# Performance work log

Hardware: AMD Instinct MI355X
Metric: run time of the kernel (lower is better)

Reference implementation:

```python
import jax, jax.numpy as jnp
import numpy as np

DIM = 256
N_EMBED = 8192
DECAY = 0.99
EPS = 1e-05


def setup_inputs() -> dict:
    key = jax.random.key(0)
    k1, k2, k3, k4 = jax.random.split(key, 4)
    z = jax.random.normal(k1, (16, 32, 32, DIM), dtype=jnp.float32)
    embedding = jax.random.normal(k2, (DIM, N_EMBED), dtype=jnp.float32)
    cluster_size = jax.random.uniform(k3, (N_EMBED,), dtype=jnp.float32)
    embedding_avg = jax.random.normal(k4, (DIM, N_EMBED), dtype=jnp.float32)
    return {"z": z, "embedding": embedding, "cluster_size": cluster_size,
            "embedding_avg": embedding_avg}


def reference(z, embedding, cluster_size, embedding_avg):
    flatten = z.reshape(-1, DIM)  # [N, dim]
    dist = ((flatten ** 2).sum(1, keepdims=True)
            - 2.0 * flatten @ embedding
            + (embedding ** 2).sum(0, keepdims=True))
    embed_ind_flat = jnp.argmin(dist, axis=1)  # [N] int
    embed_ind = embed_ind_flat.reshape(z.shape[:-1])
    # Gather codes: embedding is [dim, n_embed]; quantize [..., dim]
    quantize = jnp.take(embedding.T, embed_ind_flat, axis=0).reshape(z.shape)

    # EMA codebook update (training path), via segment sums (no dense one-hot)
    onehot_sum = jax.ops.segment_sum(
        jnp.ones_like(embed_ind_flat, dtype=flatten.dtype),
        embed_ind_flat, num_segments=N_EMBED)  # [n_embed]
    embed_sum = jax.ops.segment_sum(flatten, embed_ind_flat,
                                    num_segments=N_EMBED).T  # [dim, n_embed]
    new_cluster_size = cluster_size * DECAY + (1.0 - DECAY) * onehot_sum
    new_embedding_avg = embedding_avg * DECAY + (1.0 - DECAY) * embed_sum
    n = new_cluster_size.sum()
    smoothed = (new_cluster_size + EPS) / (n + N_EMBED * EPS) * n
    new_embedding = new_embedding_avg / smoothed[None, :]

    diff = jnp.mean((jax.lax.stop_gradient(quantize) - z) ** 2)
    quantize_st = z + jax.lax.stop_gradient(quantize - z)
    return (quantize_st, diff, embed_ind, new_embedding,
            new_cluster_size, new_embedding_avg)
```

## Files before the change

kernel.cpp:

```cpp
#include <hip/hip_runtime.h>


#define DIMC  256
#define NEMB  8192
#define NROWS 16384

#define OUT_Q      0u
#define OUT_DIFF   4194304u
#define OUT_IDX    4194305u
#define OUT_NEWEMB 4210689u
#define OUT_NEWCS  6307841u
#define OUT_NEWAVG 6316033u

#define WS_EHI    0u
#define WS_ELO    1048576u
#define WS_COUNT  2097152u
#define WS_DIFF   2105344u
#define WS_N      2105345u
#define WS_ENORM  2105346u
#define WS_PACK   2113540u

typedef __attribute__((ext_vector_type(8))) short short8;
typedef __attribute__((ext_vector_type(4))) float f32x4;

__device__ inline void split_bf16(float x, unsigned short& h, unsigned short& l) {
  unsigned u = __float_as_uint(x);
  unsigned r = u + 0x7FFFu + ((u >> 16) & 1u);
  h = (unsigned short)(r >> 16);
  float hf = __uint_as_float((unsigned)h << 16);
  float lo = x - hf;
  unsigned u2 = __float_as_uint(lo);
  unsigned r2 = u2 + 0x7FFFu + ((u2 >> 16) & 1u);
  l = (unsigned short)(r2 >> 16);
}

__device__ inline float bf16_f(unsigned short u) {
  return __uint_as_float((unsigned)u << 16);
}

__global__ __launch_bounds__(256) void prep_kernel(
    const float* __restrict__ z, const float* __restrict__ emb,
    const float* __restrict__ cs, unsigned short* __restrict__ z_hi,
    unsigned short* __restrict__ z_lo, unsigned short* __restrict__ e_hi,
    unsigned short* __restrict__ e_lo, float* __restrict__ enorm,
    float* __restrict__ embsum, unsigned long long* __restrict__ pack,
    float* __restrict__ count_diff, float* __restrict__ n_out) {
  const int b = blockIdx.x;
  const int t = threadIdx.x;
  __shared__ float tile[64][68];
  __shared__ float red[4][64];

  if (b < 1024) {
#pragma unroll
    for (int it = 0; it < 4; ++it) {
      const int idx = (b * 256 + t) + it * 262144;
      const float4 v = reinterpret_cast<const float4*>(z)[idx];
      ushort4 h, l;
      split_bf16(v.x, h.x, l.x);
      split_bf16(v.y, h.y, l.y);
      split_bf16(v.z, h.z, l.z);
      split_bf16(v.w, h.w, l.w);
      reinterpret_cast<ushort4*>(z_hi)[idx] = h;
      reinterpret_cast<ushort4*>(z_lo)[idx] = l;
    }
  } else if (b < 1536) {
    const int bb = b - 1024;
    const int n0 = (bb & 127) * 64;
    const int k0 = (bb >> 7) * 64;
    const int c4 = (t & 15) * 4;
    const int rr = t >> 4;
#pragma unroll
    for (int i = 0; i < 4; ++i) {
      const int kl = rr + i * 16;
      const float4 v = *reinterpret_cast<const float4*>(
          &emb[(size_t)(k0 + kl) * NEMB + n0 + c4]);
      *reinterpret_cast<float4*>(&tile[kl][c4]) = v;
    }
    __syncthreads();
#pragma unroll
    for (int i = 0; i < 4; ++i) {
      const int nr = rr + i * 16;
      float4 v;
      v.x = tile[c4 + 0][nr];
      v.y = tile[c4 + 1][nr];
      v.z = tile[c4 + 2][nr];
      v.w = tile[c4 + 3][nr];
      const size_t off = (size_t)(n0 + nr) * DIMC + k0 + c4;
      ushort4 h, l;
      split_bf16(v.x, h.x, l.x);
      split_bf16(v.y, h.y, l.y);
      split_bf16(v.z, h.z, l.z);
      split_bf16(v.w, h.w, l.w);
      *reinterpret_cast<ushort4*>(&e_hi[off]) = h;
      *reinterpret_cast<ushort4*>(&e_lo[off]) = l;
    }
  } else if (b < 2048) {
    const int bb = b - 1536;
    const float4 zero = {0.f, 0.f, 0.f, 0.f};
#pragma unroll
    for (int it = 0; it < 4; ++it)
      reinterpret_cast<float4*>(embsum)[bb * 1024 + t + it * 256] = zero;
  } else if (b < 2176) {
    const int l = t & 63;
    const int dg = t >> 6;
    const int e = (b - 2048) * 64 + l;
    float s = 0.f;
#pragma unroll 8
    for (int d = dg * 64; d < dg * 64 + 64; ++d) {
      const float v = emb[(size_t)d * NEMB + e];
      s = fmaf(v, v, s);
    }
    red[dg][l] = s;
    __syncthreads();
    if (dg == 0) enorm[e] = red[0][l] + red[1][l] + red[2][l] + red[3][l];
  } else if (b < 2184) {
    const int bb = b - 2176;
    const uint4 ff = {~0u, ~0u, ~0u, ~0u};
#pragma unroll
    for (int it = 0; it < 4; ++it)
      reinterpret_cast<uint4*>(pack)[bb * 1024 + t + it * 256] = ff;
  } else if (b == 2184) {
    for (int i = t; i < 8193; i += 256) count_diff[i] = 0.f;
  } else {
    float s = 0.f;
#pragma unroll
    for (int i = 0; i < 32; ++i) s += cs[t + i * 256];
#pragma unroll
    for (int off = 32; off > 0; off >>= 1) s += __shfl_down(s, off, 64);
    if ((t & 63) == 0) red[0][t >> 6] = s;
    __syncthreads();
    if (t == 0)
      n_out[0] = 0.99f * (red[0][0] + red[0][1] + red[0][2] + red[0][3]) +
                 163.84f;
  }
}

__global__ __launch_bounds__(256, 2) void argmin_mfma_kernel(
    const unsigned short* __restrict__ z_hi, const unsigned short* __restrict__ z_lo,
    const unsigned short* __restrict__ e_hi, const unsigned short* __restrict__ e_lo,
    const float* __restrict__ enorm, unsigned long long* __restrict__ pack) {
  __shared__ short za[16384];
  __shared__ short eb[16384];
  const int tid = threadIdx.x;
  const int bid = blockIdx.x;
  const int r0 = (bid >> 2) * 128;
  const int ebase = (bid & 3) * 2048;
  const int tx = tid & 15;
  const int q = (tid >> 4) & 3;
  const int wave = tid >> 6;
  const int wm = wave & 1;
  const int wn = wave >> 1;

  float rmin[4][4];
  int ridx[4][4];
#pragma unroll
  for (int i = 0; i < 4; ++i)
#pragma unroll
    for (int r = 0; r < 4; ++r) { rmin[i][r] = 3.4028235e38f; ridx[i][r] = 0; }

  for (int nt = 0; nt < 16; ++nt) {
    const int n0 = ebase + nt * 128;
    f32x4 acc[4][4];
#pragma unroll
    for (int i = 0; i < 4; ++i)
#pragma unroll
      for (int j = 0; j < 4; ++j) acc[i][j] = (f32x4)0.0f;

    for (int kt = 0; kt < 4; ++kt) {
      const int k0 = kt * 64;
      __syncthreads();
#pragma unroll
      for (int it = 0; it < 8; ++it) {
        const int P = tid + it * 256;
        const int row = P >> 4;
        const int p = P & 15;
        const int o = (p & 7) ^ (row & 7);
        const unsigned short* zsrc =
            ((p & 8) ? z_lo : z_hi) + (size_t)(r0 + row) * DIMC + k0 + o * 8;
        __builtin_amdgcn_global_load_lds(
            (const __attribute__((address_space(1))) unsigned int*)zsrc,
            (__attribute__((address_space(3))) unsigned int*)&za[P * 8], 16, 0, 0);
        const unsigned short* esrc =
            ((p & 8) ? e_lo : e_hi) + (size_t)(n0 + row) * DIMC + k0 + o * 8;
        __builtin_amdgcn_global_load_lds(
            (const __attribute__((address_space(1))) unsigned int*)esrc,
            (__attribute__((address_space(3))) unsigned int*)&eb[P * 8], 16, 0, 0);
      }
      __syncthreads();
#pragma unroll
      for (int ks = 0; ks < 2; ++ks) {
        short8 ah[4], al[4], bh[4], bl[4];
#pragma unroll
        for (int i = 0; i < 4; ++i) {
          const int rl = wm * 64 + i * 16 + tx;
          const int oa = (ks * 4 + q) ^ (rl & 7);
          ah[i] = *reinterpret_cast<const short8*>(&za[rl * 128 + oa * 8]);
          al[i] = *reinterpret_cast<const short8*>(&za[rl * 128 + (oa + 8) * 8]);
          const int cl = wn * 64 + i * 16 + tx;
          const int ob = (ks * 4 + q) ^ (cl & 7);
          bh[i] = *reinterpret_cast<const short8*>(&eb[cl * 128 + ob * 8]);
          bl[i] = *reinterpret_cast<const short8*>(&eb[cl * 128 + (ob + 8) * 8]);
        }
#pragma unroll
        for (int i = 0; i < 4; ++i)
#pragma unroll
          for (int j = 0; j < 4; ++j) {
            acc[i][j] = __builtin_amdgcn_mfma_f32_16x16x32_bf16(ah[i], bh[j],
                                                               acc[i][j], 0, 0, 0);
            acc[i][j] = __builtin_amdgcn_mfma_f32_16x16x32_bf16(ah[i], bl[j],
                                                               acc[i][j], 0, 0, 0);
            acc[i][j] = __builtin_amdgcn_mfma_f32_16x16x32_bf16(al[i], bh[j],
                                                               acc[i][j], 0, 0, 0);
          }
      }
    }
#pragma unroll
    for (int j = 0; j < 4; ++j) {
      const int col = n0 + wn * 64 + j * 16 + tx;
      const float en = enorm[col];
#pragma unroll
      for (int i = 0; i < 4; ++i)
#pragma unroll
        for (int r = 0; r < 4; ++r) {
          const float s = en - 2.0f * acc[i][j][r];
          if (s < rmin[i][r]) { rmin[i][r] = s; ridx[i][r] = col; }
        }
    }
  }
#pragma unroll
  for (int i = 0; i < 4; ++i)
#pragma unroll
    for (int r = 0; r < 4; ++r) {
      float v = rmin[i][r];
      int ix = ridx[i][r];
#pragma unroll
      for (int off = 1; off < 16; off <<= 1) {
        const float ov = __shfl_xor(v, off, 16);
        const int oi = __shfl_xor(ix, off, 16);
        if (ov < v || (ov == v && oi < ix)) { v = ov; ix = oi; }
      }
      if (tx == 0) {
        const unsigned int fb = __float_as_uint(v);
        const unsigned int sb = (fb & 0x80000000u) ? ~fb : (fb | 0x80000000u);
        const unsigned long long key =
            ((unsigned long long)sb << 13) | (unsigned long long)(unsigned)ix;
        atomicMin(&pack[r0 + wm * 64 + i * 16 + q * 4 + r], key);
      }
    }
}

__global__ __launch_bounds__(256) void gather_update_kernel(
    const float* __restrict__ z, const unsigned short* __restrict__ e_hi,
    const unsigned short* __restrict__ e_lo,
    const unsigned long long* __restrict__ pack, float* __restrict__ out_q,
    float* __restrict__ out_idx, float* __restrict__ embsum,
    float* __restrict__ count, float* __restrict__ diff_acc) {
  const int row = blockIdx.x * 4 + (threadIdx.x >> 6);
  const int lane = threadIdx.x & 63;
  const int e = (int)(pack[row] & 8191ULL);
  if (lane == 0) out_idx[row] = (float)e;
  const float4 zv =
      *reinterpret_cast<const float4*>(&z[(size_t)row * DIMC + lane * 4]);
  const ushort4 h =
      *reinterpret_cast<const ushort4*>(&e_hi[(size_t)e * DIMC + lane * 4]);
  const ushort4 l =
      *reinterpret_cast<const ushort4*>(&e_lo[(size_t)e * DIMC + lane * 4]);
  const float q0 = bf16_f(h.x) + bf16_f(l.x);
  const float q1 = bf16_f(h.y) + bf16_f(l.y);
  const float q2 = bf16_f(h.z) + bf16_f(l.z);
  const float q3 = bf16_f(h.w) + bf16_f(l.w);
  const float d0 = q0 - zv.x, d1 = q1 - zv.y, d2 = q2 - zv.z, d3 = q3 - zv.w;
  float4 st;
  st.x = zv.x + d0; st.y = zv.y + d1; st.z = zv.z + d2; st.w = zv.w + d3;
  *reinterpret_cast<float4*>(&out_q[(size_t)row * DIMC + lane * 4]) = st;

  atomicAdd(&embsum[(size_t)e * DIMC + lane * 4 + 0], zv.x);
  atomicAdd(&embsum[(size_t)e * DIMC + lane * 4 + 1], zv.y);
  atomicAdd(&embsum[(size_t)e * DIMC + lane * 4 + 2], zv.z);
  atomicAdd(&embsum[(size_t)e * DIMC + lane * 4 + 3], zv.w);

  float local = d0 * d0 + d1 * d1 + d2 * d2 + d3 * d3;
#pragma unroll
  for (int off = 32; off > 0; off >>= 1) local += __shfl_down(local, off, 64);

  __shared__ float dred[4];
  if (lane == 0) {
    dred[threadIdx.x >> 6] = local;
    atomicAdd(&count[e], 1.0f);
  }
  __syncthreads();
  if (threadIdx.x == 0)
    atomicAdd(diff_acc, dred[0] + dred[1] + dred[2] + dred[3]);
}

__global__ __launch_bounds__(256) void fin1_kernel(
    const float* __restrict__ eavg, const float* __restrict__ embsum,
    const float* __restrict__ cs, const float* __restrict__ count,
    const float* __restrict__ n_ptr, const float* __restrict__ diff_acc,
    float* __restrict__ out_emb, float* __restrict__ out_ncs,
    float* __restrict__ out_diff) {
  const int b = blockIdx.x;
  const int t = threadIdx.x;
  __shared__ float tile[64][68];
  __shared__ float rs[64];
  if (b < 512) {
    const int e0 = (b & 127) * 64;
    const int d0 = (b >> 7) * 64;
    const int c4 = (t & 15) * 4;
    const int rr = t >> 4;
    if (t < 64) {
      const float n = n_ptr[0];
      const float ncs = cs[e0 + t] * 0.99f + 0.01f * count[e0 + t];
      const float sm = (ncs + 1e-5f) / (n + 0.08192f) * n;
      rs[t] = 1.0f / sm;
    }
#pragma unroll
    for (int i = 0; i < 4; ++i) {
      const int er = rr + i * 16;
      const float4 v = *reinterpret_cast<const float4*>(
          &embsum[(size_t)(e0 + er) * DIMC + d0 + c4]);
      *reinterpret_cast<float4*>(&tile[er][c4]) = v;
    }
    __syncthreads();
#pragma unroll
    for (int i = 0; i < 4; ++i) {
      const int dr = rr + i * 16;
      const size_t g = (size_t)(d0 + dr) * NEMB + e0 + c4;
      const float4 av = *reinterpret_cast<const float4*>(&eavg[g]);
      float4 o;
      o.x = (av.x * 0.99f + 0.01f * tile[c4 + 0][dr]) * rs[c4 + 0];
      o.y = (av.y * 0.99f + 0.01f * tile[c4 + 1][dr]) * rs[c4 + 1];
      o.z = (av.z * 0.99f + 0.01f * tile[c4 + 2][dr]) * rs[c4 + 2];
      o.w = (av.w * 0.99f + 0.01f * tile[c4 + 3][dr]) * rs[c4 + 3];
      *reinterpret_cast<float4*>(&out_emb[g]) = o;
    }
  } else {
    const int g = (b - 512) * 256 + t;
    out_ncs[g] = cs[g] * 0.99f + 0.01f * count[g];
    if (g == 0) out_diff[0] = diff_acc[0] * (1.0f / 4194304.0f);
  }
}

__global__ __launch_bounds__(256) void fin2b_kernel(
    const float* __restrict__ cs, const float* __restrict__ count,
    const float* __restrict__ n_ptr, const float* __restrict__ out_emb,
    float* __restrict__ out_avg) {
  const int g = blockIdx.x * 256 + threadIdx.x;
  const int e = g & 8191;
  const float n = n_ptr[0];
  const float ncs = cs[e] * 0.99f + 0.01f * count[e];
  const float sm = (ncs + 1e-5f) / (n + 0.08192f) * n;
  out_avg[g] = out_emb[g] * sm;
}

extern "C" void kernel_launch(void* const* d_in, const int* in_sizes, int n_in,
                              void* d_out, int out_size, void* d_ws,
                              size_t ws_size, hipStream_t stream) {
  const float* z = (const float*)d_in[0];
  const float* emb = (const float*)d_in[1];
  const float* cs = (const float*)d_in[2];
  const float* eavg = (const float*)d_in[3];
  float* out = (float*)d_out;
  float* ws = (float*)d_ws;

  unsigned short* e_hi = (unsigned short*)(ws + WS_EHI);
  unsigned short* e_lo = (unsigned short*)(ws + WS_ELO);
  float* ws_count = ws + WS_COUNT;
  float* ws_diff = ws + WS_DIFF;
  float* ws_n = ws + WS_N;
  float* ws_enorm = ws + WS_ENORM;
  unsigned long long* ws_pack = (unsigned long long*)(ws + WS_PACK);

  unsigned short* z_hi = (unsigned short*)(out + OUT_Q);
  unsigned short* z_lo = (unsigned short*)(out + OUT_Q + 2097152);
  float* embsum = out + OUT_NEWAVG;

  prep_kernel<<<2186, 256, 0, stream>>>(z, emb, cs, z_hi, z_lo, e_hi, e_lo,
                                        ws_enorm, embsum, ws_pack, ws_count,
                                        ws_n);
  argmin_mfma_kernel<<<512, 256, 0, stream>>>(z_hi, z_lo, e_hi, e_lo, ws_enorm,
                                              ws_pack);
  gather_update_kernel<<<NROWS / 4, 256, 0, stream>>>(
      z, e_hi, e_lo, ws_pack, out + OUT_Q, out + OUT_IDX, embsum, ws_count,
      ws_diff);
  fin1_kernel<<<544, 256, 0, stream>>>(eavg, embsum, cs, ws_count, ws_n,
                                       ws_diff, out + OUT_NEWEMB,
                                       out + OUT_NEWCS, out + OUT_DIFF);
  fin2b_kernel<<<(DIMC * NEMB) / 256, 256, 0, stream>>>(
      cs, ws_count, ws_n, out + OUT_NEWEMB, out + OUT_NEWAVG);
}
```

Baseline: 390.0 us.

## Accumulate embed sums in dim-major layout and fuse finalize kernels

The scatter-add of z rows into the codebook sum now writes directly in [dim, n_embed] layout, so the finalize step no longer needs a shared-memory transpose. The two finalize kernels are merged into one elementwise pass that computes the new embedding average in place and the normalized embedding together, which removes one full read-back pass over the output. The price is that the atomics in the gather kernel become strided by NEMB across lanes, so each wavefront's 256 atomic adds land in separate cache lines rather than being contiguous.

```diff
diff --git a/kernel.cpp b/kernel.cpp
--- a/kernel.cpp
+++ b/kernel.cpp
@@ -253,7 +253,7 @@
     const float* __restrict__ z, const unsigned short* __restrict__ e_hi,
     const unsigned short* __restrict__ e_lo,
     const unsigned long long* __restrict__ pack, float* __restrict__ out_q,
-    float* __restrict__ out_idx, float* __restrict__ embsum,
+    float* __restrict__ out_idx, float* __restrict__ embsum_de,
     float* __restrict__ count, float* __restrict__ diff_acc) {
   const int row = blockIdx.x * 4 + (threadIdx.x >> 6);
   const int lane = threadIdx.x & 63;
@@ -274,10 +274,10 @@
   st.x = zv.x + d0; st.y = zv.y + d1; st.z = zv.z + d2; st.w = zv.w + d3;
   *reinterpret_cast<float4*>(&out_q[(size_t)row * DIMC + lane * 4]) = st;
 
-  atomicAdd(&embsum[(size_t)e * DIMC + lane * 4 + 0], zv.x);
-  atomicAdd(&embsum[(size_t)e * DIMC + lane * 4 + 1], zv.y);
-  atomicAdd(&embsum[(size_t)e * DIMC + lane * 4 + 2], zv.z);
-  atomicAdd(&embsum[(size_t)e * DIMC + lane * 4 + 3], zv.w);
+  atomicAdd(&embsum_de[(size_t)(lane * 4 + 0) * NEMB + e], zv.x);
+  atomicAdd(&embsum_de[(size_t)(lane * 4 + 1) * NEMB + e], zv.y);
+  atomicAdd(&embsum_de[(size_t)(lane * 4 + 2) * NEMB + e], zv.z);
+  atomicAdd(&embsum_de[(size_t)(lane * 4 + 3) * NEMB + e], zv.w);
 
   float local = d0 * d0 + d1 * d1 + d2 * d2 + d3 * d3;
 #pragma unroll
@@ -293,64 +293,39 @@
     atomicAdd(diff_acc, dred[0] + dred[1] + dred[2] + dred[3]);
 }
 
-__global__ __launch_bounds__(256) void fin1_kernel(
-    const float* __restrict__ eavg, const float* __restrict__ embsum,
-    const float* __restrict__ cs, const float* __restrict__ count,
-    const float* __restrict__ n_ptr, const float* __restrict__ diff_acc,
+__global__ __launch_bounds__(256) void fin_kernel(
+    const float* __restrict__ eavg, const float* __restrict__ cs,
+    const float* __restrict__ count, const float* __restrict__ n_ptr,
+    const float* __restrict__ diff_acc, float* __restrict__ avg_io,
     float* __restrict__ out_emb, float* __restrict__ out_ncs,
     float* __restrict__ out_diff) {
   const int b = blockIdx.x;
   const int t = threadIdx.x;
-  __shared__ float tile[64][68];
-  __shared__ float rs[64];
-  if (b < 512) {
-    const int e0 = (b & 127) * 64;
-    const int d0 = (b >> 7) * 64;
-    const int c4 = (t & 15) * 4;
-    const int rr = t >> 4;
-    if (t < 64) {
-      const float n = n_ptr[0];
-      const float ncs = cs[e0 + t] * 0.99f + 0.01f * count[e0 + t];
-      const float sm = (ncs + 1e-5f) / (n + 0.08192f) * n;
-      rs[t] = 1.0f / sm;
-    }
-#pragma unroll
-    for (int i = 0; i < 4; ++i) {
-      const int er = rr + i * 16;
-      const float4 v = *reinterpret_cast<const float4*>(
-          &embsum[(size_t)(e0 + er) * DIMC + d0 + c4]);
-      *reinterpret_cast<float4*>(&tile[er][c4]) = v;
-    }
-    __syncthreads();
-#pragma unroll
-    for (int i = 0; i < 4; ++i) {
-      const int dr = rr + i * 16;
-      const size_t g = (size_t)(d0 + dr) * NEMB + e0 + c4;
-      const float4 av = *reinterpret_cast<const float4*>(&eavg[g]);
-      float4 o;
-      o.x = (av.x * 0.99f + 0.01f * tile[c4 + 0][dr]) * rs[c4 + 0];
-      o.y = (av.y * 0.99f + 0.01f * tile[c4 + 1][dr]) * rs[c4 + 1];
-      o.z = (av.z * 0.99f + 0.01f * tile[c4 + 2][dr]) * rs[c4 + 2];
-      o.w = (av.w * 0.99f + 0.01f * tile[c4 + 3][dr]) * rs[c4 + 3];
-      *reinterpret_cast<float4*>(&out_emb[g]) = o;
-    }
+  if (b < 2048) {
+    const int g4 = b * 256 + t;
+    const int g = g4 * 4;
+    const int e = g & 8191;
+    const float n = n_ptr[0];
+    const float4 sv = reinterpret_cast<const float4*>(avg_io)[g4];
+    const float4 av = reinterpret_cast<const float4*>(eavg)[g4];
+    float4 avg;
+    avg.x = av.x * 0.99f + 0.01f * sv.x;
+    avg.y = av.y * 0.99f + 0.01f * sv.y;
+    avg.z = av.z * 0.99f + 0.01f * sv.z;
+    avg.w = av.w * 0.99f + 0.01f * sv.w;
+    reinterpret_cast<float4*>(avg_io)[g4] = avg;
+    const float inv_den = 1.0f / (n + 0.08192f);
+    float4 o;
+    o.x = avg.x / ((cs[e + 0] * 0.99f + 0.01f * count[e + 0] + 1e-5f) * inv_den * n);
+    o.y = avg.y / ((cs[e + 1] * 0.99f + 0.01f * count[e + 1] + 1e-5f) * inv_den * n);
+    o.z = avg.z / ((cs[e + 2] * 0.99f + 0.01f * count[e + 2] + 1e-5f) * inv_den * n);
+    o.w = avg.w / ((cs[e + 3] * 0.99f + 0.01f * count[e + 3] + 1e-5f) * inv_den * n);
+    reinterpret_cast<float4*>(out_emb)[g4] = o;
   } else {
-    const int g = (b - 512) * 256 + t;
+    const int g = (b - 2048) * 256 + t;
     out_ncs[g] = cs[g] * 0.99f + 0.01f * count[g];
     if (g == 0) out_diff[0] = diff_acc[0] * (1.0f / 4194304.0f);
   }
-}
-
-__global__ __launch_bounds__(256) void fin2b_kernel(
-    const float* __restrict__ cs, const float* __restrict__ count,
-    const float* __restrict__ n_ptr, const float* __restrict__ out_emb,
-    float* __restrict__ out_avg) {
-  const int g = blockIdx.x * 256 + threadIdx.x;
-  const int e = g & 8191;
-  const float n = n_ptr[0];
-  const float ncs = cs[e] * 0.99f + 0.01f * count[e];
-  const float sm = (ncs + 1e-5f) / (n + 0.08192f) * n;
-  out_avg[g] = out_emb[g] * sm;
 }
 
 extern "C" void kernel_launch(void* const* d_in, const int* in_sizes, int n_in,
@@ -373,19 +348,17 @@
 
   unsigned short* z_hi = (unsigned short*)(out + OUT_Q);
   unsigned short* z_lo = (unsigned short*)(out + OUT_Q + 2097152);
-  float* embsum = out + OUT_NEWAVG;
+  float* embsum_de = out + OUT_NEWAVG;
 
   prep_kernel<<<2186, 256, 0, stream>>>(z, emb, cs, z_hi, z_lo, e_hi, e_lo,
-                                        ws_enorm, embsum, ws_pack, ws_count,
+                                        ws_enorm, embsum_de, ws_pack, ws_count,
                                         ws_n);
   argmin_mfma_kernel<<<512, 256, 0, stream>>>(z_hi, z_lo, e_hi, e_lo, ws_enorm,
                                               ws_pack);
   gather_update_kernel<<<NROWS / 4, 256, 0, stream>>>(
-      z, e_hi, e_lo, ws_pack, out + OUT_Q, out + OUT_IDX, embsum, ws_count,
+      z, e_hi, e_lo, ws_pack, out + OUT_Q, out + OUT_IDX, embsum_de, ws_count,
       ws_diff);
-  fin1_kernel<<<544, 256, 0, stream>>>(eavg, embsum, cs, ws_count, ws_n,
-                                       ws_diff, out + OUT_NEWEMB,
+  fin_kernel<<<2080, 256, 0, stream>>>(eavg, cs, ws_count, ws_n, ws_diff,
+                                       embsum_de, out + OUT_NEWEMB,
                                        out + OUT_NEWCS, out + OUT_DIFF);
-  fin2b_kernel<<<(DIMC * NEMB) / 256, 256, 0, stream>>>(
-      cs, ws_count, ws_n, out + OUT_NEWEMB, out + OUT_NEWAVG);
-}
+}
```

Result: slower. 511.3 us (+31.1%).
